# Kernel tuning notes

Measured on AMD Instinct MI355X. Metric: run time of the kernel, lower is better.

## Reference

```python
import jax, jax.numpy as jnp
import numpy as np

D = 128
N = 50000    # nodes in bond graph g
E = 500000   # edges in g == nodes in line graph lg
ELG = 500000 # edges in line graph lg


def _linear_params(key, d_in, d_out):
    k1, k2 = jax.random.split(key)
    s = 1.0 / np.sqrt(d_in)
    W = jax.random.uniform(k1, (d_in, d_out), jnp.float32, -s, s)
    b = jax.random.uniform(k2, (d_out,), jnp.float32, -s, s)
    return W, b


def setup_inputs() -> dict:
    key = jax.random.key(0)
    ks = jax.random.split(key, 32)
    inp = {
        'x': jax.random.normal(ks[0], (N, D), jnp.float32),
        'edge_x': jax.random.normal(ks[1], (E, D), jnp.float32),
        'lg_edge_attr': jax.random.normal(ks[2], (ELG, D), jnp.float32),
        'g_edge_index': jax.random.randint(ks[3], (2, E), 0, N),
        'lg_edge_index': jax.random.randint(ks[4], (2, ELG), 0, E),
    }
    i = 5
    for pre in ('eu', 'nu'):
        for nm in ('sg', 'dg', 'eg', 'su', 'du'):
            W, b = _linear_params(ks[i], D, D); i += 1
            inp[pre + '_W' + nm] = W
            inp[pre + '_b' + nm] = b
        inp[pre + '_gamma'] = jnp.ones((D,), jnp.float32)
        inp[pre + '_beta'] = jnp.zeros((D,), jnp.float32)
    return inp


def _layernorm(x, g, b):
    m = jnp.mean(x, -1, keepdims=True)
    v = jnp.var(x, -1, keepdims=True)
    return (x - m) * jax.lax.rsqrt(v + 1e-5) * g + b


def _egc(x, edge_index, edge_attr,
         Wsg, bsg, Wdg, bdg, Weg, beg, Wsu, bsu, Wdu, bdu, gamma, beta):
    # Edge-gated graph conv. PyG convention: x_i = x[dst], x_j = x[src],
    # aggregate messages at dst (edge_index[1]).
    src, dst = edge_index[0], edge_index[1]
    # Project once at node level, then gather (same math as gather-then-linear).
    sg = x @ Wsg + bsg          # src_gate(x_i) precomputed per node
    dg = x @ Wdg + bdg          # dst_gate(x_j)
    du = x @ Wdu + bdu          # dst_update(x_j)
    gate = jax.nn.silu(sg[dst] + dg[src] + edge_attr @ Weg + beg)  # [E, D]
    msg = gate * du[src]                                           # [E, D]
    aggr = jax.ops.segment_sum(msg, dst, num_segments=x.shape[0])  # [N, D]
    out = jax.nn.silu(_layernorm(x @ Wsu + bsu + aggr, gamma, beta))
    return out + x  # residual (in_channels == out_channels here)


def reference(x, edge_x, lg_edge_attr,
              eu_Wsg, eu_bsg, eu_Wdg, eu_bdg, eu_Weg, eu_beg,
              eu_Wsu, eu_bsu, eu_Wdu, eu_bdu, eu_gamma, eu_beta,
              nu_Wsg, nu_bsg, nu_Wdg, nu_bdg, nu_Weg, nu_beg,
              nu_Wsu, nu_bsu, nu_Wdu, nu_bdu, nu_gamma, nu_beta,
              g_edge_index, lg_edge_index):
    # 1) edge update on line graph (lg nodes are g's edges)
    ea = _egc(edge_x, lg_edge_index, lg_edge_attr,
              eu_Wsg, eu_bsg, eu_Wdg, eu_bdg, eu_Weg, eu_beg,
              eu_Wsu, eu_bsu, eu_Wdu, eu_bdu, eu_gamma, eu_beta)
    # 2) node update on bond graph using updated edge features
    xn = _egc(x, g_edge_index, ea,
              nu_Wsg, nu_bsg, nu_Wdg, nu_bdg, nu_Weg, nu_beg,
              nu_Wsu, nu_bsu, nu_Wdu, nu_bdu, nu_gamma, nu_beta)
    return (xn, ea)
```

## Files before the change

### kernel.cpp

```cpp
#include <hip/hip_runtime.h>
#include <stdint.h>

#define DD 128

typedef __bf16 bf16x8 __attribute__((ext_vector_type(8)));
typedef float f32x4 __attribute__((ext_vector_type(4)));
typedef unsigned short u16;
typedef u16 u16x8 __attribute__((ext_vector_type(8)));

__device__ __forceinline__ u16 f2bf(float f) {
  union { __bf16 h; u16 u; } v; v.h = (__bf16)f; return v.u;
}
__device__ __forceinline__ float bf2f(u16 b) {
  union { uint32_t u; float f; } v; v.u = (uint32_t)b << 16; return v.f;
}
__device__ __forceinline__ float silu_f(float x) {
  return x / (1.0f + __expf(-x));
}
__device__ __forceinline__ uint32_t pkbf(float lo, float hi) {
  return (uint32_t)f2bf(lo) | ((uint32_t)f2bf(hi) << 16);
}

struct ARegs { float4 v[8][2]; };

__device__ __forceinline__ void issue_A(ARegs& r, const float* __restrict__ src,
                                        int base, int M, int tid) {
#pragma unroll
  for (int i = 0; i < 8; ++i) {
    int id = tid + (i << 8);
    int row = id >> 4;
    int cc = id & 15;
    if (base + row < M) {
      const float4* p = (const float4*)(src + (size_t)(base + row) * DD + cc * 8);
      r.v[i][0] = p[0]; r.v[i][1] = p[1];
    } else {
      r.v[i][0] = make_float4(0.f, 0.f, 0.f, 0.f);
      r.v[i][1] = make_float4(0.f, 0.f, 0.f, 0.f);
    }
  }
}

__device__ __forceinline__ void write_A(u16* Ab, const ARegs& r, int tid) {
#pragma unroll
  for (int i = 0; i < 8; ++i) {
    int id = tid + (i << 8);
    int row = id >> 4;
    int cc = id & 15;
    u16x8 o;
    o[0] = f2bf(r.v[i][0].x); o[1] = f2bf(r.v[i][0].y);
    o[2] = f2bf(r.v[i][0].z); o[3] = f2bf(r.v[i][0].w);
    o[4] = f2bf(r.v[i][1].x); o[5] = f2bf(r.v[i][1].y);
    o[6] = f2bf(r.v[i][1].z); o[7] = f2bf(r.v[i][1].w);
    *(u16x8*)&Ab[row * DD + ((cc ^ (row & 7)) << 3)] = o;
  }
}

__device__ __forceinline__ void mma_stage(const u16* Ab, const u16* __restrict__ wt,
                                          f32x4 acc[4][4], int lane, int wr, int wc) {
  int g = lane >> 4, r15 = lane & 15, s = r15 & 7;
  const u16* wbase = wt + (size_t)(wc * 64 + r15) * DD;
#pragma unroll
  for (int kk = 0; kk < 4; ++kk) {
    int ko = ((kk << 2) | g) << 3;
    bf16x8 bfr[4];
#pragma unroll
    for (int n = 0; n < 4; ++n)
      bfr[n] = *(const bf16x8*)&wbase[n * 16 * DD + ko];
    bf16x8 af[4];
#pragma unroll
    for (int m = 0; m < 4; ++m) {
      int rr = wr * 64 + m * 16 + r15;
      af[m] = *(const bf16x8*)&Ab[rr * DD + ((((kk << 2) | g) ^ s) << 3)];
    }
#pragma unroll
    for (int m = 0; m < 4; ++m)
#pragma unroll
      for (int n = 0; n < 4; ++n)
        acc[m][n] = __builtin_amdgcn_mfma_f32_16x16x32_bf16(af[m], bfr[n], acc[m][n], 0, 0, 0);
  }
}

__device__ __forceinline__ void zero_acc(f32x4 a[4][4]) {
  const f32x4 z4 = {0.f, 0.f, 0.f, 0.f};
#pragma unroll
  for (int m = 0; m < 4; ++m)
#pragma unroll
    for (int n = 0; n < 4; ++n) a[m][n] = z4;
}

__device__ __forceinline__ void store_acc(const f32x4 acc[4][4], u16* __restrict__ out,
                                          size_t rs, int co, int base, int M,
                                          int lane, int wr, int wc,
                                          const float* biasS) {
  int l15 = lane & 15;
  bool oddl = lane & 1;
#pragma unroll
  for (int m = 0; m < 4; ++m) {
    int rb = wr * 64 + m * 16 + ((lane >> 4) << 2);
#pragma unroll
    for (int j = 0; j < 4; ++j) {
      int row = rb + j;
      bool act = (base + row < M);
      size_t rowoff = (size_t)(base + row) * rs + co;
#pragma unroll
      for (int n0 = 0; n0 < 4; n0 += 2) {
        int c0 = wc * 64 + n0 * 16 + l15;
        int c1 = c0 + 16;
        float v0 = acc[m][n0][j] + (biasS ? biasS[c0] : 0.f);
        float v1 = acc[m][n0 + 1][j] + (biasS ? biasS[c1] : 0.f);
        float t0 = __shfl_xor(v0, 1);
        float t1 = __shfl_xor(v1, 1);
        uint32_t pk = oddl ? pkbf(t1, v1) : pkbf(v0, t0);
        int col2 = oddl ? (c1 - 1) : c0;
        if (act) *(uint32_t*)&out[rowoff + col2] = pk;
      }
    }
  }
}

template <bool FOUR>
__global__ void __launch_bounds__(256, 2) proj_kernel(
    int M, const float* __restrict__ src, const u16* __restrict__ wt,
    const float* __restrict__ bsg, const float* __restrict__ bdg,
    const float* __restrict__ beg, const float* __restrict__ bdu,
    const float* __restrict__ bsu,
    u16* __restrict__ o_sg, u16* __restrict__ o_dgdu, u16* __restrict__ o_su) {
  __shared__ u16 Ab[128 * DD];
  __shared__ float bSg[DD], bDu[DD], bSu[DD];
  int tid = threadIdx.x, lane = tid & 63, wid = tid >> 6;
  int wr = wid >> 1, wc = wid & 1;
  int base = blockIdx.x * 128;
  if (FOUR && tid < 128) {
    bSg[tid] = bsg[tid] + bdg[tid] + beg[tid];
    bDu[tid] = bdu[tid];
    bSu[tid] = bsu[tid];
  }
  {
    ARegs ar;
    issue_A(ar, src, base, M, tid);
    write_A(Ab, ar, tid);
  }
  __syncthreads();
  f32x4 acc[4][4];
  zero_acc(acc);
  mma_stage(Ab, wt + 0 * 16384, acc, lane, wr, wc);
  store_acc(acc, o_sg, DD, 0, base, M, lane, wr, wc, FOUR ? bSg : nullptr);
  if (FOUR) {
    zero_acc(acc);
    mma_stage(Ab, wt + 1 * 16384, acc, lane, wr, wc);
    store_acc(acc, o_dgdu, 2 * DD, 0, base, M, lane, wr, wc, nullptr);
    zero_acc(acc);
    mma_stage(Ab, wt + 3 * 16384, acc, lane, wr, wc);
    store_acc(acc, o_dgdu, 2 * DD, DD, base, M, lane, wr, wc, bDu);
    zero_acc(acc);
    mma_stage(Ab, wt + 4 * 16384, acc, lane, wr, wc);
    store_acc(acc, o_su, DD, 0, base, M, lane, wr, wc, bSu);
  }
}

__global__ void __launch_bounds__(256) hist_kernel(const int* __restrict__ dst,
                                                   int Me, int* __restrict__ cnt) {
  int i = blockIdx.x * blockDim.x + threadIdx.x;
  if (i < Me) atomicAdd(&cnt[dst[i]], 1);
}

__global__ void __launch_bounds__(256) scan1_kernel(const int* __restrict__ cnt, int M,
                                                    int* __restrict__ out,
                                                    int* __restrict__ bsum) {
  __shared__ int sh[256];
  int t = threadIdx.x;
  int i0 = blockIdx.x * 1024 + t * 4;
  int v[4];
#pragma unroll
  for (int k = 0; k < 4; ++k) v[k] = (i0 + k < M) ? cnt[i0 + k] : 0;
  int s = v[0] + v[1] + v[2] + v[3];
  sh[t] = s;
  __syncthreads();
#pragma unroll
  for (int off = 1; off < 256; off <<= 1) {
    int x = (t >= off) ? sh[t - off] : 0;
    __syncthreads();
    sh[t] += x;
    __syncthreads();
  }
  int run = sh[t] - s;
  if (t == 255) bsum[blockIdx.x] = sh[255];
#pragma unroll
  for (int k = 0; k < 4; ++k) {
    if (i0 + k < M) out[i0 + k] = run;
    run += v[k];
  }
}

__global__ void __launch_bounds__(256) scan2_kernel(int* __restrict__ bsum, int NB) {
  __shared__ int sh[512];
  int t = threadIdx.x;
  for (int i = t; i < 512; i += 256) sh[i] = (i < NB) ? bsum[i] : 0;
  __syncthreads();
  for (int off = 1; off < 512; off <<= 1) {
    int tmp[2];
#pragma unroll
    for (int q = 0; q < 2; ++q) {
      int i = t + q * 256;
      tmp[q] = (i >= off) ? sh[i - off] : 0;
    }
    __syncthreads();
#pragma unroll
    for (int q = 0; q < 2; ++q) sh[t + q * 256] += tmp[q];
    __syncthreads();
  }
  for (int i = t; i < NB; i += 256) bsum[i] = (i == 0) ? 0 : sh[i - 1];
}

__global__ void __launch_bounds__(256) scan3_kernel(int* __restrict__ rowptr,
                                                    const int* __restrict__ bscan,
                                                    int M, int Medges,
                                                    int* __restrict__ head) {
  int i = blockIdx.x * blockDim.x + threadIdx.x;
  if (i < M) {
    int v = rowptr[i] + bscan[i >> 10];
    rowptr[i] = v;
    head[i] = v;
  }
  if (i == 0) rowptr[M] = Medges;
}

__global__ void __launch_bounds__(256) eid_kernel(const int* __restrict__ src,
                                                  const int* __restrict__ dst, int Me,
                                                  int* __restrict__ head,
                                                  int* __restrict__ eids,
                                                  int* __restrict__ srcs) {
  int i = blockIdx.x * blockDim.x + threadIdx.x;
  if (i < Me) {
    int s = atomicAdd(&head[dst[i]], 1);
    eids[s] = i;
    srcs[s] = src[i];
  }
}

__global__ void prep_weights(const float* __restrict__ w0, const float* __restrict__ w1,
                             const float* __restrict__ w2, const float* __restrict__ w3,
                             const float* __restrict__ w4, const float* __restrict__ w5,
                             const float* __restrict__ w6, const float* __restrict__ w7,
                             const float* __restrict__ w8, const float* __restrict__ w9,
                             u16* __restrict__ wt) {
  const float* W;
  switch (blockIdx.x) {
    case 0: W = w0; break; case 1: W = w1; break; case 2: W = w2; break;
    case 3: W = w3; break; case 4: W = w4; break; case 5: W = w5; break;
    case 6: W = w6; break; case 7: W = w7; break; case 8: W = w8; break;
    default: W = w9; break;
  }
  u16* dst = wt + blockIdx.x * 16384;
  for (int o = threadIdx.x; o < 16384; o += 256) {
    int n = o >> 7, k = o & 127;
    dst[o] = f2bf(W[k * DD + n]);
  }
}

__global__ void __launch_bounds__(256) gfin_kernel(
    int M, const int* __restrict__ rptr, const int* __restrict__ eids,
    const int* __restrict__ srcs,
    const u16* __restrict__ sg_t, const u16* __restrict__ dgdu_t,
    const u16* __restrict__ su_t, const u16* __restrict__ egp,
    const float* __restrict__ gamma, const float* __restrict__ beta,
    const float* __restrict__ resid, float* __restrict__ out) {
  int gtid = blockIdx.x * blockDim.x + threadIdx.x;
  int r = gtid >> 4;
  int l16 = gtid & 15;
  if (r >= M) return;
  int c = l16 * 8;

  u16x8 sgp = *(const u16x8*)&sg_t[(size_t)r * DD + c];
  float sg[8], ax[8];
#pragma unroll
  for (int k = 0; k < 8; ++k) { sg[k] = bf2f(sgp[k]); ax[k] = 0.f; }

  int segb = rptr[r], sege = rptr[r + 1];
  for (int s = segb; s < sege; ++s) {
    int e = eids[s];
    int sv = srcs[s];
    u16x8 gp = *(const u16x8*)&egp[(size_t)e * DD + c];
    u16x8 dgp = *(const u16x8*)&dgdu_t[(size_t)sv * (2 * DD) + c];
    u16x8 dup = *(const u16x8*)&dgdu_t[(size_t)sv * (2 * DD) + DD + c];
#pragma unroll
    for (int k = 0; k < 8; ++k) {
      float g = silu_f(sg[k] + bf2f(dgp[k]) + bf2f(gp[k]));
      ax[k] += g * bf2f(dup[k]);
    }
  }

  u16x8 sup = *(const u16x8*)&su_t[(size_t)r * DD + c];
  float v[8];
  float sum = 0.f;
#pragma unroll
  for (int k = 0; k < 8; ++k) { v[k] = bf2f(sup[k]) + ax[k]; sum += v[k]; }
#pragma unroll
  for (int off = 1; off <= 8; off <<= 1) sum += __shfl_xor(sum, off);
  float mean = sum * (1.0f / 128.0f);
  float sq = 0.f;
#pragma unroll
  for (int k = 0; k < 8; ++k) { v[k] -= mean; sq += v[k] * v[k]; }
#pragma unroll
  for (int off = 1; off <= 8; off <<= 1) sq += __shfl_xor(sq, off);
  float rs = rsqrtf(sq * (1.0f / 128.0f) + 1e-5f);

  float4 gm0 = *(const float4*)&gamma[c];
  float4 gm1 = *(const float4*)&gamma[c + 4];
  float4 bt0 = *(const float4*)&beta[c];
  float4 bt1 = *(const float4*)&beta[c + 4];
  float4 rr0 = *(const float4*)&resid[(size_t)r * DD + c];
  float4 rr1 = *(const float4*)&resid[(size_t)r * DD + c + 4];
  float gmv[8] = {gm0.x, gm0.y, gm0.z, gm0.w, gm1.x, gm1.y, gm1.z, gm1.w};
  float btv[8] = {bt0.x, bt0.y, bt0.z, bt0.w, bt1.x, bt1.y, bt1.z, bt1.w};
  float rrv[8] = {rr0.x, rr0.y, rr0.z, rr0.w, rr1.x, rr1.y, rr1.z, rr1.w};
  float o[8];
#pragma unroll
  for (int k = 0; k < 8; ++k)
    o[k] = silu_f(v[k] * rs * gmv[k] + btv[k]) + rrv[k];
  float4 o0 = {o[0], o[1], o[2], o[3]};
  float4 o1 = {o[4], o[5], o[6], o[7]};
  *(float4*)&out[(size_t)r * DD + c] = o0;
  *(float4*)&out[(size_t)r * DD + c + 4] = o1;
}

extern "C" void kernel_launch(void* const* d_in, const int* in_sizes, int n_in,
                              void* d_out, int out_size, void* d_ws, size_t ws_size,
                              hipStream_t stream) {
  const float* x   = (const float*)d_in[0];
  const float* ex  = (const float*)d_in[1];
  const float* lga = (const float*)d_in[2];
  const int* gei   = (const int*)d_in[3];
  const int* lgei  = (const int*)d_in[4];
  int N   = in_sizes[0] / DD;
  int E   = in_sizes[3] / 2;
  int ELG = in_sizes[4] / 2;

  char* p = (char*)d_ws;
  size_t off = 0;
  auto alloc = [&](size_t bytes) { char* q = p + off; off += (bytes + 255) & ~255ull; return q; };

  u16* wt     = (u16*)alloc((size_t)10 * 16384 * 2);
  u16* sgE    = (u16*)alloc((size_t)E * DD * 2);
  u16* dgduE  = (u16*)alloc((size_t)E * 2 * DD * 2);
  u16* suE    = (u16*)alloc((size_t)E * DD * 2);
  int  maxME  = (ELG > E) ? ELG : E;
  u16* egpB   = (u16*)alloc((size_t)maxME * DD * 2);
  u16* sgN    = (u16*)alloc((size_t)N * DD * 2);
  u16* dgduN  = (u16*)alloc((size_t)N * 2 * DD * 2);
  u16* suN    = (u16*)alloc((size_t)N * DD * 2);
  int* cnt_e  = (int*)alloc((size_t)E * 4);
  int* rptr_e = (int*)alloc((size_t)(E + 1) * 4);
  int* head_e = (int*)alloc((size_t)E * 4);
  int* eids_e = (int*)alloc((size_t)ELG * 4);
  int* srcs_e = (int*)alloc((size_t)ELG * 4);
  int* cnt_n  = (int*)alloc((size_t)N * 4);
  int* rptr_n = (int*)alloc((size_t)(N + 1) * 4);
  int* head_n = (int*)alloc((size_t)N * 4);
  int* eids_n = (int*)alloc((size_t)E * 4);
  int* srcs_n = (int*)alloc((size_t)E * 4);
  int* bsum   = (int*)alloc(512 * 4);
  if (ws_size < off) return;

  float* xn_out = (float*)d_out;
  float* ea_out = (float*)d_out + (size_t)N * DD;

  prep_weights<<<10, 256, 0, stream>>>(
      (const float*)d_in[5], (const float*)d_in[7], (const float*)d_in[9],
      (const float*)d_in[13], (const float*)d_in[11],
      (const float*)d_in[17], (const float*)d_in[19], (const float*)d_in[21],
      (const float*)d_in[25], (const float*)d_in[23], wt);

  hipMemsetAsync(cnt_e, 0, (size_t)E * 4, stream);
  hipMemsetAsync(cnt_n, 0, (size_t)N * 4, stream);
  hist_kernel<<<(ELG + 255) / 256, 256, 0, stream>>>(lgei + ELG, ELG, cnt_e);
  hist_kernel<<<(E + 255) / 256, 256, 0, stream>>>(gei + E, E, cnt_n);

  int NBe = (E + 1023) / 1024;
  scan1_kernel<<<NBe, 256, 0, stream>>>(cnt_e, E, rptr_e, bsum);
  scan2_kernel<<<1, 256, 0, stream>>>(bsum, NBe);
  scan3_kernel<<<(E + 255) / 256, 256, 0, stream>>>(rptr_e, bsum, E, ELG, head_e);
  eid_kernel<<<(ELG + 255) / 256, 256, 0, stream>>>(lgei, lgei + ELG, ELG, head_e,
                                                    eids_e, srcs_e);

  int NBn = (N + 1023) / 1024;
  scan1_kernel<<<NBn, 256, 0, stream>>>(cnt_n, N, rptr_n, bsum);
  scan2_kernel<<<1, 256, 0, stream>>>(bsum, NBn);
  scan3_kernel<<<(N + 255) / 256, 256, 0, stream>>>(rptr_n, bsum, N, E, head_n);
  eid_kernel<<<(E + 255) / 256, 256, 0, stream>>>(gei, gei + E, E, head_n,
                                                  eids_n, srcs_n);

  proj_kernel<true><<<(E + 127) / 128, 256, 0, stream>>>(
      E, ex, wt,
      (const float*)d_in[6], (const float*)d_in[8], (const float*)d_in[10],
      (const float*)d_in[14], (const float*)d_in[12],
      sgE, dgduE, suE);
  proj_kernel<false><<<(ELG + 127) / 128, 256, 0, stream>>>(
      ELG, lga, wt + 2 * 16384,
      nullptr, nullptr, nullptr, nullptr, nullptr,
      egpB, nullptr, nullptr);
  gfin_kernel<<<(E + 15) / 16, 256, 0, stream>>>(
      E, rptr_e, eids_e, srcs_e, sgE, dgduE, suE, egpB,
      (const float*)d_in[15], (const float*)d_in[16], ex, ea_out);

  proj_kernel<true><<<(N + 127) / 128, 256, 0, stream>>>(
      N, x, wt + 5 * 16384,
      (const float*)d_in[18], (const float*)d_in[20], (const float*)d_in[22],
      (const float*)d_in[26], (const float*)d_in[24],
      sgN, dgduN, suN);
  proj_kernel<false><<<(E + 127) / 128, 256, 0, stream>>>(
      E, ea_out, wt + 7 * 16384,
      nullptr, nullptr, nullptr, nullptr, nullptr,
      egpB, nullptr, nullptr);
  gfin_kernel<<<(N + 15) / 16, 256, 0, stream>>>(
      N, rptr_n, eids_n, srcs_n, sgN, dgduN, suN, egpB,
      (const float*)d_in[27], (const float*)d_in[28], x, xn_out);
}
```

Baseline: 929.1 us.

## Make projection GEMM persistent with double-buffered A tile prefetch and bias-initialized accumulators

The projection kernel becomes persistent: a grid of at most 512 blocks loops over 128-row tiles. The next tile's fp32 input is loaded into registers while the current tile's MFMAs run, then written into a second LDS buffer. Biases are folded once by a small kernel and used to initialize the accumulators, which removes the per-element bias add in the store path. The cost is doubled LDS per block (64KB), which may limit occupancy against the requested 2 blocks per CU, plus extra register pressure from holding the prefetch registers.

Measured after the change: 1.284 ms. 1.38x slower.

```diff
diff --git a/kernel.cpp b/kernel.cpp
--- a/kernel.cpp
+++ b/kernel.cpp
@@ -80,18 +80,21 @@
   }
 }
 
-__device__ __forceinline__ void zero_acc(f32x4 a[4][4]) {
-  const f32x4 z4 = {0.f, 0.f, 0.f, 0.f};
-#pragma unroll
-  for (int m = 0; m < 4; ++m)
-#pragma unroll
-    for (int n = 0; n < 4; ++n) a[m][n] = z4;
+__device__ __forceinline__ void init_acc(f32x4 a[4][4], const float* __restrict__ bias,
+                                         int lane, int wc) {
+  int l15 = lane & 15;
+#pragma unroll
+  for (int n = 0; n < 4; ++n) {
+    float b = bias ? bias[wc * 64 + n * 16 + l15] : 0.f;
+    f32x4 v = {b, b, b, b};
+#pragma unroll
+    for (int m = 0; m < 4; ++m) a[m][n] = v;
+  }
 }
 
 __device__ __forceinline__ void store_acc(const f32x4 acc[4][4], u16* __restrict__ out,
                                           size_t rs, int co, int base, int M,
-                                          int lane, int wr, int wc,
-                                          const float* biasS) {
+                                          int lane, int wr, int wc) {
   int l15 = lane & 15;
   bool oddl = lane & 1;
 #pragma unroll
@@ -105,13 +108,12 @@
 #pragma unroll
       for (int n0 = 0; n0 < 4; n0 += 2) {
         int c0 = wc * 64 + n0 * 16 + l15;
-        int c1 = c0 + 16;
-        float v0 = acc[m][n0][j] + (biasS ? biasS[c0] : 0.f);
-        float v1 = acc[m][n0 + 1][j] + (biasS ? biasS[c1] : 0.f);
+        float v0 = acc[m][n0][j];
+        float v1 = acc[m][n0 + 1][j];
         float t0 = __shfl_xor(v0, 1);
         float t1 = __shfl_xor(v1, 1);
         uint32_t pk = oddl ? pkbf(t1, v1) : pkbf(v0, t0);
-        int col2 = oddl ? (c1 - 1) : c0;
+        int col2 = oddl ? (c0 + 15) : c0;
         if (act) *(uint32_t*)&out[rowoff + col2] = pk;
       }
     }
@@ -120,41 +122,44 @@
 
 template <bool FOUR>
 __global__ void __launch_bounds__(256, 2) proj_kernel(
-    int M, const float* __restrict__ src, const u16* __restrict__ wt,
-    const float* __restrict__ bsg, const float* __restrict__ bdg,
-    const float* __restrict__ beg, const float* __restrict__ bdu,
-    const float* __restrict__ bsu,
+    int M, int ntiles, const float* __restrict__ src, const u16* __restrict__ wt,
+    const float* __restrict__ bF,
     u16* __restrict__ o_sg, u16* __restrict__ o_dgdu, u16* __restrict__ o_su) {
-  __shared__ u16 Ab[128 * DD];
-  __shared__ float bSg[DD], bDu[DD], bSu[DD];
+  __shared__ u16 Ab[2][128 * DD];
   int tid = threadIdx.x, lane = tid & 63, wid = tid >> 6;
   int wr = wid >> 1, wc = wid & 1;
-  int base = blockIdx.x * 128;
-  if (FOUR && tid < 128) {
-    bSg[tid] = bsg[tid] + bdg[tid] + beg[tid];
-    bDu[tid] = bdu[tid];
-    bSu[tid] = bsu[tid];
-  }
-  {
-    ARegs ar;
-    issue_A(ar, src, base, M, tid);
-    write_A(Ab, ar, tid);
-  }
-  __syncthreads();
+  int G = (int)gridDim.x;
+  int t = blockIdx.x;
+  ARegs ar;
+  issue_A(ar, src, t * 128, M, tid);
+  write_A(Ab[0], ar, tid);
+  int cur = 0;
   f32x4 acc[4][4];
-  zero_acc(acc);
-  mma_stage(Ab, wt + 0 * 16384, acc, lane, wr, wc);
-  store_acc(acc, o_sg, DD, 0, base, M, lane, wr, wc, FOUR ? bSg : nullptr);
-  if (FOUR) {
-    zero_acc(acc);
-    mma_stage(Ab, wt + 1 * 16384, acc, lane, wr, wc);
-    store_acc(acc, o_dgdu, 2 * DD, 0, base, M, lane, wr, wc, nullptr);
-    zero_acc(acc);
-    mma_stage(Ab, wt + 3 * 16384, acc, lane, wr, wc);
-    store_acc(acc, o_dgdu, 2 * DD, DD, base, M, lane, wr, wc, bDu);
-    zero_acc(acc);
-    mma_stage(Ab, wt + 4 * 16384, acc, lane, wr, wc);
-    store_acc(acc, o_su, DD, 0, base, M, lane, wr, wc, bSu);
+  for (;;) {
+    int tn = t + G;
+    bool more = (tn < ntiles);
+    if (more) issue_A(ar, src, tn * 128, M, tid);
+    __syncthreads();
+    const u16* A = Ab[cur];
+    int base = t * 128;
+    init_acc(acc, FOUR ? bF : nullptr, lane, wc);
+    mma_stage(A, wt + 0 * 16384, acc, lane, wr, wc);
+    store_acc(acc, o_sg, DD, 0, base, M, lane, wr, wc);
+    if (FOUR) {
+      init_acc(acc, nullptr, lane, wc);
+      mma_stage(A, wt + 1 * 16384, acc, lane, wr, wc);
+      store_acc(acc, o_dgdu, 2 * DD, 0, base, M, lane, wr, wc);
+      init_acc(acc, bF + 128, lane, wc);
+      mma_stage(A, wt + 3 * 16384, acc, lane, wr, wc);
+      store_acc(acc, o_dgdu, 2 * DD, DD, base, M, lane, wr, wc);
+      init_acc(acc, bF + 256, lane, wc);
+      mma_stage(A, wt + 4 * 16384, acc, lane, wr, wc);
+      store_acc(acc, o_su, DD, 0, base, M, lane, wr, wc);
+    }
+    if (!more) break;
+    write_A(Ab[cur ^ 1], ar, tid);
+    cur ^= 1;
+    t = tn;
   }
 }
 
@@ -258,6 +263,23 @@
   }
 }
 
+__global__ void fold_bias(const float* __restrict__ e_sg, const float* __restrict__ e_dg,
+                          const float* __restrict__ e_eg, const float* __restrict__ e_du,
+                          const float* __restrict__ e_su,
+                          const float* __restrict__ n_sg, const float* __restrict__ n_dg,
+                          const float* __restrict__ n_eg, const float* __restrict__ n_du,
+                          const float* __restrict__ n_su, float* __restrict__ out) {
+  int i = threadIdx.x;
+  if (i < 128) {
+    out[i]        = e_sg[i] + e_dg[i] + e_eg[i];
+    out[128 + i]  = e_du[i];
+    out[256 + i]  = e_su[i];
+    out[384 + i]  = n_sg[i] + n_dg[i] + n_eg[i];
+    out[512 + i]  = n_du[i];
+    out[640 + i]  = n_su[i];
+  }
+}
+
 __global__ void __launch_bounds__(256) gfin_kernel(
     int M, const int* __restrict__ rptr, const int* __restrict__ eids,
     const int* __restrict__ srcs,
@@ -341,6 +363,7 @@
   auto alloc = [&](size_t bytes) { char* q = p + off; off += (bytes + 255) & ~255ull; return q; };
 
   u16* wt     = (u16*)alloc((size_t)10 * 16384 * 2);
+  float* biasF = (float*)alloc(768 * 4);
   u16* sgE    = (u16*)alloc((size_t)E * DD * 2);
   u16* dgduE  = (u16*)alloc((size_t)E * 2 * DD * 2);
   u16* suE    = (u16*)alloc((size_t)E * DD * 2);
@@ -370,6 +393,11 @@
       (const float*)d_in[13], (const float*)d_in[11],
       (const float*)d_in[17], (const float*)d_in[19], (const float*)d_in[21],
       (const float*)d_in[25], (const float*)d_in[23], wt);
+  fold_bias<<<1, 128, 0, stream>>>(
+      (const float*)d_in[6], (const float*)d_in[8], (const float*)d_in[10],
+      (const float*)d_in[14], (const float*)d_in[12],
+      (const float*)d_in[18], (const float*)d_in[20], (const float*)d_in[22],
+      (const float*)d_in[26], (const float*)d_in[24], biasF);
 
   hipMemsetAsync(cnt_e, 0, (size_t)E * 4, stream);
   hipMemsetAsync(cnt_n, 0, (size_t)N * 4, stream);
@@ -390,28 +418,23 @@
   eid_kernel<<<(E + 255) / 256, 256, 0, stream>>>(gei, gei + E, E, head_n,
                                                   eids_n, srcs_n);
 
-  proj_kernel<true><<<(E + 127) / 128, 256, 0, stream>>>(
-      E, ex, wt,
-      (const float*)d_in[6], (const float*)d_in[8], (const float*)d_in[10],
-      (const float*)d_in[14], (const float*)d_in[12],
-      sgE, dgduE, suE);
-  proj_kernel<false><<<(ELG + 127) / 128, 256, 0, stream>>>(
-      ELG, lga, wt + 2 * 16384,
-      nullptr, nullptr, nullptr, nullptr, nullptr,
-      egpB, nullptr, nullptr);
+  const int PG = 512;
+  int ntE = (E + 127) / 128;   int gE = ntE < PG ? ntE : PG;
+  int ntLG = (ELG + 127) / 128; int gLG = ntLG < PG ? ntLG : PG;
+  int ntN = (N + 127) / 128;   int gN = ntN < PG ? ntN : PG;
+
+  proj_kernel<true><<<gE, 256, 0, stream>>>(
+      E, ntE, ex, wt, biasF, sgE, dgduE, suE);
+  proj_kernel<false><<<gLG, 256, 0, stream>>>(
+      ELG, ntLG, lga, wt + 2 * 16384, nullptr, egpB, nullptr, nullptr);
   gfin_kernel<<<(E + 15) / 16, 256, 0, stream>>>(
       E, rptr_e, eids_e, srcs_e, sgE, dgduE, suE, egpB,
       (const float*)d_in[15], (const float*)d_in[16], ex, ea_out);
 
-  proj_kernel<true><<<(N + 127) / 128, 256, 0, stream>>>(
-      N, x, wt + 5 * 16384,
-      (const float*)d_in[18], (const float*)d_in[20], (const float*)d_in[22],
-      (const float*)d_in[26], (const float*)d_in[24],
-      sgN, dgduN, suN);
-  proj_kernel<false><<<(E + 127) / 128, 256, 0, stream>>>(
-      E, ea_out, wt + 7 * 16384,
-      nullptr, nullptr, nullptr, nullptr, nullptr,
-      egpB, nullptr, nullptr);
+  proj_kernel<true><<<gN, 256, 0, stream>>>(
+      N, ntN, x, wt + 5 * 16384, biasF + 384, sgN, dgduN, suN);
+  proj_kernel<false><<<gE, 256, 0, stream>>>(
+      E, ntE, ea_out, wt + 7 * 16384, nullptr, egpB, nullptr, nullptr);
   gfin_kernel<<<(N + 15) / 16, 256, 0, stream>>>(
       N, rptr_n, eids_n, srcs_n, sgN, dgduN, suN, egpB,
       (const float*)d_in[27], (const float*)d_in[28], x, xn_out);
```
